# Kernel optimization log

Hardware: AMD Instinct MI355X
Metric: run time of the kernel (lower is better)

Reference implementation:

```python
import jax, jax.numpy as jnp
import numpy as np

N = 50000
E = 600000
FEAT = 32
ACT = 8
H = 128
HEADS = 4
C = H // HEADS
L = 3
NEG_SLOPE = 0.2
LN_EPS = 1e-5


def setup_inputs() -> dict:
    key = jax.random.key(0)
    ks = jax.random.split(key, 32)
    s = 0.05
    inp = {
        'x': jax.random.normal(ks[0], (N, FEAT), jnp.float32),
        'action': jax.random.normal(ks[1], (N, ACT), jnp.float32),
        'edge_index': jax.random.randint(ks[2], (2, E), 0, N, jnp.int32),
        # node encoder: Linear(feat+act -> H) + LayerNorm
        'W0': jax.random.normal(ks[3], (FEAT + ACT, H), jnp.float32) * s,
        'b0': jnp.zeros((H,), jnp.float32),
        'ln0_g': jnp.ones((H,), jnp.float32),
        'ln0_b': jnp.zeros((H,), jnp.float32),
        # GAT layers (stacked over L): lin W [L,H,heads*C], att vectors, bias, LayerNorm
        'Wg': jax.random.normal(ks[4], (L, H, HEADS * C), jnp.float32) * s,
        'att_src': jax.random.normal(ks[5], (L, HEADS, C), jnp.float32) * s,
        'att_dst': jax.random.normal(ks[6], (L, HEADS, C), jnp.float32) * s,
        'bg': jnp.zeros((L, HEADS * C), jnp.float32),
        'lng_g': jnp.ones((L, H), jnp.float32),
        'lng_b': jnp.zeros((L, H), jnp.float32),
        # dynamics head
        'Wd1': jax.random.normal(ks[7], (H, H), jnp.float32) * s,
        'bd1': jnp.zeros((H,), jnp.float32),
        'Wd2': jax.random.normal(ks[8], (H, FEAT), jnp.float32) * s,
        'bd2': jnp.zeros((FEAT,), jnp.float32),
        # reward head
        'Wr1': jax.random.normal(ks[9], (H, H // 2), jnp.float32) * s,
        'br1': jnp.zeros((H // 2,), jnp.float32),
        'Wr2': jax.random.normal(ks[10], (H // 2, 1), jnp.float32) * s,
        'br2': jnp.zeros((1,), jnp.float32),
        # constraint head
        'Wc1': jax.random.normal(ks[11], (H, H // 2), jnp.float32) * s,
        'bc1': jnp.zeros((H // 2,), jnp.float32),
        'Wc2': jax.random.normal(ks[12], (H // 2, 1), jnp.float32) * s,
        'bc2': jnp.zeros((1,), jnp.float32),
    }
    return inp


def _layernorm(x, g, b):
    mu = jnp.mean(x, axis=-1, keepdims=True)
    var = jnp.mean(jnp.square(x - mu), axis=-1, keepdims=True)
    return (x - mu) * jax.lax.rsqrt(var + LN_EPS) * g + b


def _gat_layer(h, src, dst, W, a_src, a_dst, bias):
    # PyG GATConv: xp = lin(h) per head; alpha = leaky_relu(a_src.x_j + a_dst.x_i)
    xp = (h @ W).reshape(N, HEADS, C)                    # [N, heads, C]
    s_src = jnp.sum(xp * a_src, axis=-1)                 # [N, heads]
    s_dst = jnp.sum(xp * a_dst, axis=-1)                 # [N, heads]
    alpha = jax.nn.leaky_relu(s_src[src] + s_dst[dst], NEG_SLOPE)  # [E', heads]
    # segment softmax over edges grouped by destination node
    amax = jax.ops.segment_max(alpha, dst, num_segments=N)
    ex = jnp.exp(alpha - amax[dst])
    den = jax.ops.segment_sum(ex, dst, num_segments=N)
    attn = ex / den[dst]                                 # [E', heads]
    msg = xp[src] * attn[..., None]                      # [E', heads, C]
    out = jax.ops.segment_sum(msg.reshape(-1, HEADS * C), dst, num_segments=N)
    return out + bias                                    # [N, H]


def reference(x, action, edge_index, W0, b0, ln0_g, ln0_b, Wg, att_src, att_dst,
              bg, lng_g, lng_b, Wd1, bd1, Wd2, bd2, Wr1, br1, Wr2, br2,
              Wc1, bc1, Wc2, bc2):
    # add self loops (PyG GATConv default)
    loops = jnp.arange(N, dtype=edge_index.dtype)
    src = jnp.concatenate([edge_index[0], loops])
    dst = jnp.concatenate([edge_index[1], loops])

    h = jax.nn.relu(_layernorm(jnp.concatenate([x, action], axis=-1) @ W0 + b0, ln0_g, ln0_b))
    for l in range(L):
        h_new = _gat_layer(h, src, dst, Wg[l], att_src[l], att_dst[l], bg[l])
        h_new = jax.nn.relu(_layernorm(h_new, lng_g[l], lng_b[l]))
        h = h + h_new

    delta_x = jax.nn.relu(h @ Wd1 + bd1) @ Wd2 + bd2
    next_x = x + delta_x
    graph_emb = jnp.mean(h, axis=0, keepdims=True)       # global_mean_pool, single graph
    reward = (jax.nn.relu(graph_emb @ Wr1 + br1) @ Wr2 + br2).squeeze(-1)
    constraint_prob = jax.nn.sigmoid(jax.nn.relu(graph_emb @ Wc1 + bc1) @ Wc2 + bc2).squeeze(-1)
    return delta_x, next_x, reward, constraint_prob
```

## Files before the change

### kernel.cpp

```cpp
#include <hip/hip_runtime.h>

typedef unsigned short u16;
typedef __attribute__((ext_vector_type(8))) short bf16x8;
typedef __attribute__((ext_vector_type(4))) float f32x4;

#define NN 50000
#define EE 600000
#define EP 650000
#define LNEPS 1e-5f
#define NB 196
#define ENCB 1563
#define CNTB 2540

__device__ __forceinline__ float bf2f(u16 u) {
    union { unsigned int i; float f; } v; v.i = ((unsigned int)u) << 16; return v.f;
}
__device__ __forceinline__ u16 f2bf(float f) {
    union { float f; unsigned int i; } v; v.f = f;
    unsigned int x = v.i;
    unsigned int r = x + 0x7fffu + ((x >> 16) & 1u);
    return (u16)(r >> 16);
}
__device__ __forceinline__ float ldf(const void* p, long i, int bf) {
    return bf ? bf2f(((const u16*)p)[i]) : ((const float*)p)[i];
}
__device__ __forceinline__ void stf(void* p, long i, int bf, float v) {
    if (bf) ((u16*)p)[i] = f2bf(v); else ((float*)p)[i] = v;
}

#define WTOT 93858
#define BSWN 65536
struct P22 { const void* p[22]; };

__global__ __launch_bounds__(256) void init7(P22 w, float* __restrict__ wf,
                                             u16* __restrict__ bsw,
                                             int* __restrict__ deg,
                                             float* __restrict__ gacc,
                                             int* __restrict__ flag) {
    const unsigned w0 = *(const unsigned*)w.p[2];
    const int bf = (w0 == 0x3F803F80u) ? 1 : 0;
    int i = blockIdx.x * 256 + threadIdx.x;
    if (i < WTOT) {
        const int offs[23] = {0,5120,5248,5376,5504,54656,55040,55424,55808,56192,56576,
                              72960,73088,77184,77216,85408,85472,85536,85537,93729,93793,
                              93857,93858};
        int seg = 0;
        while (offs[seg + 1] <= i) ++seg;
        wf[i] = ldf(w.p[seg], i - offs[seg], bf);
        return;
    }
    i -= WTOT;
    if (i < BSWN) {
        int mat = i >> 14, rem = i & 16383;
        int ct = rem >> 11, r2 = rem & 2047;
        int kb = r2 >> 9, r3 = r2 & 511;
        int lane = r3 >> 3, j = r3 & 7;
        int k = kb * 32 + (lane >> 4) * 8 + j;
        int n = ct * 16 + (lane & 15);
        float v = (mat < 3) ? ldf(w.p[4], (long)mat * 16384 + (long)k * 128 + n, bf)
                            : ldf(w.p[10], (long)k * 128 + n, bf);
        bsw[i] = f2bf(v);
        return;
    }
    i -= BSWN;
    if (i < NN) { deg[i] = 0; return; }
    i -= NN;
    if (i < 128) { gacc[i] = 0.f; return; }
    if (i == 128) *flag = bf;
}

__global__ __launch_bounds__(256) void enc7(
    const void* __restrict__ x, const void* __restrict__ act,
    const float* __restrict__ wf, u16* __restrict__ hb,
    const int* __restrict__ flg, const int* __restrict__ ei,
    int* __restrict__ deg) {
    if (blockIdx.x >= ENCB) {
        int e = (blockIdx.x - ENCB) * 256 + threadIdx.x;
        if (e < EP) {
            int d = (e < EE) ? ei[EE + e] : (e - EE);
            atomicAdd(&deg[d], 1);
        }
        return;
    }
    const float* W0f = wf;
    const float* b0f = wf + 5120;
    const float* gf  = wf + 5248;
    const float* bbf = wf + 5376;
    __shared__ float As[32][41];
    const int bf = *flg;
    int t = threadIdx.x;
    int r0 = blockIdx.x * 32;
    #pragma unroll
    for (int i = 0; i < 5; ++i) {
        int idx = t + i * 256;
        int r = idx / 40, k = idx - r * 40;
        int rr = r0 + r; if (rr >= NN) rr = NN - 1;
        As[r][k] = (k < 32) ? ldf(x, (long)rr * 32 + k, bf)
                            : ldf(act, (long)rr * 8 + (k - 32), bf);
    }
    __syncthreads();
    int colq = t & 31, mq = t >> 5;
    int col0 = colq * 4;
    float4 b0v = *(const float4*)(b0f + col0);
    float acc[4][4];
    #pragma unroll
    for (int j = 0; j < 4; ++j) {
        acc[j][0] = b0v.x; acc[j][1] = b0v.y; acc[j][2] = b0v.z; acc[j][3] = b0v.w;
    }
    #pragma unroll 2
    for (int k = 0; k < 40; ++k) {
        float4 b4 = *(const float4*)(W0f + k * 128 + col0);
        float a0 = As[mq * 4 + 0][k];
        float a1 = As[mq * 4 + 1][k];
        float a2 = As[mq * 4 + 2][k];
        float a3 = As[mq * 4 + 3][k];
        acc[0][0] += a0 * b4.x; acc[0][1] += a0 * b4.y; acc[0][2] += a0 * b4.z; acc[0][3] += a0 * b4.w;
        acc[1][0] += a1 * b4.x; acc[1][1] += a1 * b4.y; acc[1][2] += a1 * b4.z; acc[1][3] += a1 * b4.w;
        acc[2][0] += a2 * b4.x; acc[2][1] += a2 * b4.y; acc[2][2] += a2 * b4.z; acc[2][3] += a2 * b4.w;
        acc[3][0] += a3 * b4.x; acc[3][1] += a3 * b4.y; acc[3][2] += a3 * b4.z; acc[3][3] += a3 * b4.w;
    }
    float4 gv = *(const float4*)(gf + col0);
    float4 bv = *(const float4*)(bbf + col0);
    #pragma unroll
    for (int j = 0; j < 4; ++j) {
        int row = r0 + mq * 4 + j;
        float pa = acc[j][0] + acc[j][1] + acc[j][2] + acc[j][3];
        #pragma unroll
        for (int o = 1; o <= 16; o <<= 1) pa += __shfl_xor(pa, o, 32);
        float mu = pa * (1.f / 128.f);
        float d0 = acc[j][0] - mu, d1 = acc[j][1] - mu;
        float d2 = acc[j][2] - mu, d3 = acc[j][3] - mu;
        float q = d0 * d0 + d1 * d1 + d2 * d2 + d3 * d3;
        #pragma unroll
        for (int o = 1; o <= 16; o <<= 1) q += __shfl_xor(q, o, 32);
        float rs = rsqrtf(q * (1.f / 128.f) + LNEPS);
        if (row < NN) {
            ushort4 hbv;
            hbv.x = f2bf(fmaxf(d0 * rs * gv.x + bv.x, 0.f));
            hbv.y = f2bf(fmaxf(d1 * rs * gv.y + bv.y, 0.f));
            hbv.z = f2bf(fmaxf(d2 * rs * gv.z + bv.z, 0.f));
            hbv.w = f2bf(fmaxf(d3 * rs * gv.w + bv.w, 0.f));
            *(ushort4*)(hb + (long)row * 128 + col0) = hbv;
        }
    }
}

__global__ __launch_bounds__(256) void lin7(
    const u16* __restrict__ hb, const u16* __restrict__ bswm,
    const float* __restrict__ bias, u16* __restrict__ out, int dorelu,
    int doscore, const float* __restrict__ wf, int layer,
    float* __restrict__ s_src, float* __restrict__ s_dst,
    int douth, const void* __restrict__ x, void* __restrict__ dout,
    const int* __restrict__ flg) {
    __shared__ u16 As[32 * 136];
    __shared__ u16 ts[32 * 136];
    int t = threadIdx.x;
    int r0 = blockIdx.x * 32;
    #pragma unroll
    for (int i = 0; i < 2; ++i) {
        int idx = (t + i * 256) * 8;
        int r = idx >> 7, k = idx & 127;
        int rr = r0 + r; if (rr >= NN) rr = NN - 1;
        int4 v = *(const int4*)(hb + (long)rr * 128 + k);
        *(int4*)(As + r * 136 + k) = v;
    }
    __syncthreads();
    int w = t >> 6, lane = t & 63;
    int rt = w & 1, ctbase = (w >> 1) * 4;
    int quad = lane >> 4, l15 = lane & 15;
    int rowl = rt * 16 + l15;
    bf16x8 afr[4];
    #pragma unroll
    for (int kb = 0; kb < 4; ++kb)
        afr[kb] = *(const bf16x8*)(As + rowl * 136 + kb * 32 + quad * 8);
    const float* asrf = wf + 54656 + layer * 128;
    const float* adsf = wf + 55040 + layer * 128;
    int headbase = (w >> 1) * 2;
    #pragma unroll
    for (int cp = 0; cp < 2; ++cp) {
        int ct0 = ctbase + cp * 2, ct1 = ct0 + 1;
        f32x4 acc0 = {0.f, 0.f, 0.f, 0.f};
        f32x4 acc1 = {0.f, 0.f, 0.f, 0.f};
        #pragma unroll
        for (int kb = 0; kb < 4; ++kb) {
            bf16x8 b0 = *(const bf16x8*)(bswm + ct0 * 2048 + kb * 512 + lane * 8);
            acc0 = __builtin_amdgcn_mfma_f32_16x16x32_bf16(afr[kb], b0, acc0, 0, 0, 0);
        }
        #pragma unroll
        for (int kb = 0; kb < 4; ++kb) {
            bf16x8 b1 = *(const bf16x8*)(bswm + ct1 * 2048 + kb * 512 + lane * 8);
            acc1 = __builtin_amdgcn_mfma_f32_16x16x32_bf16(afr[kb], b1, acc1, 0, 0, 0);
        }
        int col0 = ct0 * 16 + l15, col1 = ct1 * 16 + l15;
        float bia0 = dorelu ? bias[col0] : 0.f;
        float bia1 = dorelu ? bias[col1] : 0.f;
        #pragma unroll
        for (int reg = 0; reg < 4; ++reg) {
            int lrow = rt * 16 + quad * 4 + reg;
            int grow = r0 + lrow;
            float z0 = acc0[reg] + bia0, z1 = acc1[reg] + bia1;
            if (dorelu) { z0 = fmaxf(z0, 0.f); z1 = fmaxf(z1, 0.f); }
            if (douth) {
                ts[lrow * 136 + col0] = f2bf(z0);
                ts[lrow * 136 + col1] = f2bf(z1);
            } else if (grow < NN) {
                out[(long)grow * 128 + col0] = f2bf(z0);
                out[(long)grow * 128 + col1] = f2bf(z1);
            }
        }
        if (doscore) {
            float av0 = asrf[col0], av1 = asrf[col1];
            float dv0 = adsf[col0], dv1 = adsf[col1];
            #pragma unroll
            for (int reg = 0; reg < 4; ++reg) {
                float pa = acc0[reg] * av0 + acc1[reg] * av1;
                float pb = acc0[reg] * dv0 + acc1[reg] * dv1;
                #pragma unroll
                for (int o = 1; o <= 8; o <<= 1) {
                    pa += __shfl_xor(pa, o, 64);
                    pb += __shfl_xor(pb, o, 64);
                }
                if (l15 == 0) {
                    int grow = r0 + rt * 16 + quad * 4 + reg;
                    if (grow < NN) {
                        s_src[grow * 4 + headbase + cp] = pa;
                        s_dst[grow * 4 + headbase + cp] = pb;
                    }
                }
            }
        }
    }
    if (douth) {
        __syncthreads();
        const float* Wd2f = wf + 73088;
        const float* bd2f = wf + 77184;
        const int bf = *flg;
        int c = t & 31, mq = t >> 5;
        float acc[4];
        #pragma unroll
        for (int j = 0; j < 4; ++j) acc[j] = bd2f[c];
        #pragma unroll 4
        for (int k = 0; k < 128; ++k) {
            float wv = Wd2f[k * 32 + c];
            acc[0] += bf2f(ts[(mq * 4 + 0) * 136 + k]) * wv;
            acc[1] += bf2f(ts[(mq * 4 + 1) * 136 + k]) * wv;
            acc[2] += bf2f(ts[(mq * 4 + 2) * 136 + k]) * wv;
            acc[3] += bf2f(ts[(mq * 4 + 3) * 136 + k]) * wv;
        }
        #pragma unroll
        for (int j = 0; j < 4; ++j) {
            int node = r0 + mq * 4 + j;
            if (node >= NN) continue;
            stf(dout, (long)node * 32 + c, bf, acc[j]);
            stf(dout, (long)NN * 32 + (long)node * 32 + c, bf,
                ldf(x, (long)node * 32 + c, bf) + acc[j]);
        }
    }
}

__global__ __launch_bounds__(256) void scanA(const int* __restrict__ deg,
                                             int* __restrict__ bsum) {
    __shared__ int red[256];
    int t = threadIdx.x; int i = blockIdx.x * 256 + t;
    red[t] = (i < NN) ? deg[i] : 0; __syncthreads();
    for (int s = 128; s >= 1; s >>= 1) { if (t < s) red[t] += red[t + s]; __syncthreads(); }
    if (t == 0) bsum[blockIdx.x] = red[0];
}

__global__ __launch_bounds__(256) void scanC2(const int* __restrict__ deg,
                                              const int* __restrict__ bsum,
                                              int* __restrict__ offs,
                                              int* __restrict__ cursor) {
    __shared__ int sh[256];
    int t = threadIdx.x;
    sh[t] = (t < NB) ? bsum[t] : 0;
    __syncthreads();
    for (int o = 1; o < 256; o <<= 1) {
        int u = (t >= o) ? sh[t - o] : 0;
        __syncthreads();
        sh[t] += u;
        __syncthreads();
    }
    int pre = (blockIdx.x == 0) ? 0 : sh[blockIdx.x - 1];
    __syncthreads();
    int i = blockIdx.x * 256 + t;
    int v = (i < NN) ? deg[i] : 0;
    sh[t] = v;
    __syncthreads();
    for (int o = 1; o < 256; o <<= 1) {
        int u = (t >= o) ? sh[t - o] : 0;
        __syncthreads();
        sh[t] += u;
        __syncthreads();
    }
    if (i < NN) {
        int excl = pre + sh[t] - v;
        offs[i] = excl; cursor[i] = excl;
    }
    if (i == 0) offs[NN] = EP;
}

__global__ void scatter5(const int* __restrict__ ei, int* __restrict__ cursor,
                         int* __restrict__ csrc) {
    int e = blockIdx.x * 256 + threadIdx.x; if (e >= EP) return;
    int s, d;
    if (e < EE) { s = ei[e]; d = ei[EE + e]; } else { s = e - EE; d = s; }
    int p = atomicAdd(&cursor[d], 1);
    csrc[p] = s;
}

__global__ __launch_bounds__(256) void agg10(
    const u16* __restrict__ xp, const float* __restrict__ s_src,
    const float* __restrict__ s_dst,
    const int* __restrict__ csrc, const int* __restrict__ offs,
    const float* __restrict__ wf, int layer, u16* __restrict__ hb) {
    const float* bgf = wf + 55424 + layer * 128;
    const float* gf  = wf + 55808 + layer * 128;
    const float* bbf = wf + 56192 + layer * 128;
    int t = threadIdx.x;
    int lane = t & 63;
    int n = blockIdx.x * 4 + (t >> 6);
    int q = (lane >> 4) & 3;
    int l16 = lane & 15;
    int c0 = l16 * 8;
    int hd = l16 >> 2;
    long idx0 = (long)n * 128 + c0;
    int4 hold = *(const int4*)(hb + idx0);
    float sdn = s_dst[n * 4 + (lane & 3)];
    int beg = offs[n], end = offs[n + 1];
    float a[8] = {};
    float den = 0.f;
    for (int cbeg = beg; cbeg < end; cbeg += 64) {
        int cdeg = end - cbeg; if (cdeg > 64) cdeg = 64;
        int eidx = (lane < cdeg) ? csrc[cbeg + lane] : n;
        for (int base = 0; base < cdeg; base += 16) {
            int me = base + (lane >> 2);
            int sm = __shfl(eidx, me & 63, 64);
            float aw = s_src[sm * 4 + (lane & 3)] + sdn;
            aw = (aw > 0.f) ? aw : 0.2f * aw;
            float wv = (me < cdeg) ? __expf(aw) : 0.f;
            int s00 = __shfl(eidx, base + q, 64);
            int s01 = __shfl(eidx, base + 4 + q, 64);
            int s10 = __shfl(eidx, base + 8 + q, 64);
            int s11 = __shfl(eidx, base + 12 + q, 64);
            int4 v00 = *(const int4*)(xp + (long)s00 * 128 + c0);
            int4 v01 = *(const int4*)(xp + (long)s01 * 128 + c0);
            int4 v10 = *(const int4*)(xp + (long)s10 * 128 + c0);
            int4 v11 = *(const int4*)(xp + (long)s11 * 128 + c0);
            float w00 = __shfl(wv, (q << 2) | hd, 64);
            float w01 = __shfl(wv, ((4 + q) << 2) | hd, 64);
            float w10 = __shfl(wv, ((8 + q) << 2) | hd, 64);
            float w11 = __shfl(wv, ((12 + q) << 2) | hd, 64);
            union { int4 i; u16 u[8]; } u00, u01, u10, u11;
            u00.i = v00; u01.i = v01; u10.i = v10; u11.i = v11;
            #pragma unroll
            for (int k = 0; k < 8; ++k)
                a[k] += w00 * bf2f(u00.u[k]) + w01 * bf2f(u01.u[k])
                      + w10 * bf2f(u10.u[k]) + w11 * bf2f(u11.u[k]);
            den += w00 + w01 + w10 + w11;
        }
    }
    #pragma unroll
    for (int k = 0; k < 8; ++k) {
        a[k] += __shfl_xor(a[k], 16, 64);
        a[k] += __shfl_xor(a[k], 32, 64);
    }
    den += __shfl_xor(den, 16, 64);
    den += __shfl_xor(den, 32, 64);
    float inv = 1.f / den;
    float4 bg0 = *(const float4*)(bgf + c0);
    float4 bg1 = *(const float4*)(bgf + c0 + 4);
    float v[8];
    v[0] = a[0] * inv + bg0.x; v[1] = a[1] * inv + bg0.y;
    v[2] = a[2] * inv + bg0.z; v[3] = a[3] * inv + bg0.w;
    v[4] = a[4] * inv + bg1.x; v[5] = a[5] * inv + bg1.y;
    v[6] = a[6] * inv + bg1.z; v[7] = a[7] * inv + bg1.w;
    float pa = v[0] + v[1] + v[2] + v[3] + v[4] + v[5] + v[6] + v[7];
    #pragma unroll
    for (int o = 1; o <= 8; o <<= 1) pa += __shfl_xor(pa, o, 16);
    float mu = pa * (1.f / 128.f);
    float d[8];
    float qv = 0.f;
    #pragma unroll
    for (int k = 0; k < 8; ++k) { d[k] = v[k] - mu; qv += d[k] * d[k]; }
    #pragma unroll
    for (int o = 1; o <= 8; o <<= 1) qv += __shfl_xor(qv, o, 16);
    float rs = rsqrtf(qv * (1.f / 128.f) + LNEPS);
    float4 g0 = *(const float4*)(gf + c0);
    float4 g1 = *(const float4*)(gf + c0 + 4);
    float4 b0 = *(const float4*)(bbf + c0);
    float4 b1 = *(const float4*)(bbf + c0 + 4);
    float gg[8]  = {g0.x, g0.y, g0.z, g0.w, g1.x, g1.y, g1.z, g1.w};
    float bbv[8] = {b0.x, b0.y, b0.z, b0.w, b1.x, b1.y, b1.z, b1.w};
    if (lane < 16) {
        union { int4 i; u16 u[8]; } hv, ho;
        ho.i = hold;
        #pragma unroll
        for (int k = 0; k < 8; ++k) {
            float y = fmaxf(d[k] * rs * gg[k] + bbv[k], 0.f);
            hv.u[k] = f2bf(bf2f(ho.u[k]) + y);
        }
        *(int4*)(hb + idx0) = hv.i;
    }
}

__global__ __launch_bounds__(128) void pool4(const u16* __restrict__ hb, float* __restrict__ gacc) {
    int c = threadIdx.x;
    int n0 = blockIdx.x * 128;
    float s = 0.f;
    for (int i = 0; i < 128; ++i) {
        int n = n0 + i;
        if (n < NN) s += bf2f(hb[(long)n * 128 + c]);
    }
    atomicAdd(&gacc[c], s);
}

__global__ __launch_bounds__(128) void head4(
    const float* __restrict__ gacc, const float* __restrict__ wf,
    void* __restrict__ out, const int* __restrict__ flg) {
    const float* Wr1f = wf + 77216;
    const float* br1f = wf + 85408;
    const float* Wr2f = wf + 85472;
    const float* br2f = wf + 85536;
    const float* Wc1f = wf + 85537;
    const float* bc1f = wf + 93729;
    const float* Wc2f = wf + 93793;
    const float* bc2f = wf + 93857;
    __shared__ float ge[128];
    __shared__ float hr[128];
    const int bf = *flg;
    int t = threadIdx.x;
    ge[t] = gacc[t] * (1.f / (float)NN);
    __syncthreads();
    {
        int j = t & 63;
        const float* W = (t < 64) ? Wr1f : Wc1f;
        const float* bb = (t < 64) ? br1f : bc1f;
        float a = bb[j];
        for (int k = 0; k < 128; ++k) a += ge[k] * W[k * 64 + j];
        hr[t] = fmaxf(a, 0.f);
    }
    __syncthreads();
    if (t == 0) {
        float r = br2f[0];
        for (int j = 0; j < 64; ++j) r += hr[j] * Wr2f[j];
        stf(out, (long)2 * NN * 32, bf, r);
    } else if (t == 1) {
        float z = bc2f[0];
        for (int j = 0; j < 64; ++j) z += hr[64 + j] * Wc2f[j];
        float p = 1.f / (1.f + __expf(-z));
        stf(out, (long)2 * NN * 32 + 1, bf, p);
    }
}

extern "C" void kernel_launch(void* const* d_in, const int* in_sizes, int n_in,
                              void* d_out, int out_size, void* d_ws, size_t ws_size,
                              hipStream_t stream) {
    const void* x   = d_in[0];
    const void* act = d_in[1];
    const int*  ei  = (const int*)d_in[2];

    char* ws = (char*)d_ws;
    size_t off = 0;
    auto alloc = [&](size_t bytes) -> char* {
        char* p = ws + off;
        off = (off + bytes + 255) & ~(size_t)255;
        return p;
    };
    u16*       hb     = (u16*)      alloc((size_t)NN * 128 * 2);
    u16*       xp     = (u16*)      alloc((size_t)NN * 128 * 2);
    float*     s_src  = (float*)    alloc((size_t)NN * 4 * 4);
    float*     s_dst  = (float*)    alloc((size_t)NN * 4 * 4);
    int*       deg    = (int*)      alloc((size_t)NN * 4);
    int*       cursor = (int*)      alloc((size_t)NN * 4);
    int*       offs   = (int*)      alloc((size_t)(NN + 1) * 4);
    int*       csrc   = (int*)      alloc((size_t)EP * 4);
    float*     wf     = (float*)    alloc((size_t)WTOT * 4);
    u16*       bsw    = (u16*)      alloc((size_t)BSWN * 2);
    float*     gacc   = (float*)    alloc(128 * 4);
    int*       flag   = (int*)      alloc(4);
    int*       bsum   = (int*)      alloc((size_t)NB * 4);
    int*       boff   = (int*)      alloc((size_t)NB * 4);
    (void)boff;

    P22 wp;
    for (int i = 0; i < 22; ++i) wp.p[i] = d_in[3 + i];
    const int initN = WTOT + BSWN + NN + 129;
    init7<<<(initN + 255) / 256, 256, 0, stream>>>(wp, wf, bsw, deg, gacc, flag);

    enc7<<<ENCB + CNTB, 256, 0, stream>>>(x, act, wf, hb, flag, ei, deg);

    scanA<<<NB, 256, 0, stream>>>(deg, bsum);
    scanC2<<<NB, 256, 0, stream>>>(deg, bsum, offs, cursor);
    scatter5<<<(EP + 255) / 256, 256, 0, stream>>>(ei, cursor, csrc);

    for (int l = 0; l < 3; ++l) {
        lin7<<<ENCB, 256, 0, stream>>>(hb, bsw + (size_t)l * 16384,
                                       (const float*)nullptr, xp, 0,
                                       1, wf, l, s_src, s_dst,
                                       0, x, d_out, flag);
        agg10<<<NN / 4, 256, 0, stream>>>(xp, s_src, s_dst, csrc, offs,
                                          wf, l, hb);
    }

    lin7<<<ENCB, 256, 0, stream>>>(hb, bsw + (size_t)3 * 16384,
                                   wf + 72960, xp, 1,
                                   0, wf, 0, s_src, s_dst,
                                   1, x, d_out, flag);

    pool4<<<(NN + 127) / 128, 128, 0, stream>>>(hb, gacc);
    head4<<<1, 128, 0, stream>>>(gacc, wf, d_out, flag);

    (void)in_sizes; (void)n_in; (void)out_size; (void)ws_size;
}
```

Before: 413.3 us.

## Fuse CSR scatter into first GAT linear and pooling into final head linear

The edge scatter that builds the CSR source list now runs as extra blocks inside the first layer's linear kernel, and the global mean-pool partial sums are computed from the shared-memory tile in the final linear kernel. Pooling goes into 16 striped accumulators to spread the atomic traffic, and the head kernel sums them. This removes two kernel launches and a separate pass over the hidden state, at the cost of more atomics inside the final linear and a larger grid for the first linear.

Measured after the change: 377.7 us. -8.6%, faster.

```diff
diff --git a/kernel.cpp b/kernel.cpp
--- a/kernel.cpp
+++ b/kernel.cpp
@@ -65,8 +65,8 @@
     i -= BSWN;
     if (i < NN) { deg[i] = 0; return; }
     i -= NN;
-    if (i < 128) { gacc[i] = 0.f; return; }
-    if (i == 128) *flag = bf;
+    if (i < 2048) { gacc[i] = 0.f; return; }
+    if (i == 2048) *flag = bf;
 }
 
 __global__ __launch_bounds__(256) void enc7(
@@ -145,15 +145,28 @@
     }
 }
 
-__global__ __launch_bounds__(256) void lin7(
+__global__ __launch_bounds__(256) void lin8(
     const u16* __restrict__ hb, const u16* __restrict__ bswm,
     const float* __restrict__ bias, u16* __restrict__ out, int dorelu,
     int doscore, const float* __restrict__ wf, int layer,
     float* __restrict__ s_src, float* __restrict__ s_dst,
     int douth, const void* __restrict__ x, void* __restrict__ dout,
-    const int* __restrict__ flg) {
+    const int* __restrict__ flg,
+    int doscatter, const int* __restrict__ ei, int* __restrict__ cursor,
+    int* __restrict__ csrc, float* __restrict__ gacc) {
+    if (doscatter && blockIdx.x >= ENCB) {
+        int e = (blockIdx.x - ENCB) * 256 + threadIdx.x;
+        if (e < EP) {
+            int s, d;
+            if (e < EE) { s = ei[e]; d = ei[EE + e]; } else { s = e - EE; d = s; }
+            int p = atomicAdd(&cursor[d], 1);
+            csrc[p] = s;
+        }
+        return;
+    }
     __shared__ u16 As[32 * 136];
     __shared__ u16 ts[32 * 136];
+    __shared__ float ps[128];
     int t = threadIdx.x;
     int r0 = blockIdx.x * 32;
     #pragma unroll
@@ -255,6 +268,15 @@
             stf(dout, (long)NN * 32 + (long)node * 32 + c, bf,
                 ldf(x, (long)node * 32 + c, bf) + acc[j]);
         }
+        int pc = t & 127, half = t >> 7;
+        float s = 0.f;
+        #pragma unroll
+        for (int r2 = half * 16; r2 < half * 16 + 16; ++r2) {
+            if (r0 + r2 < NN) s += bf2f(As[r2 * 136 + pc]);
+        }
+        if (half == 0) ps[pc] = s;
+        __syncthreads();
+        if (half == 1) atomicAdd(&gacc[(blockIdx.x & 15) * 128 + pc], s + ps[pc]);
     }
 }
 
@@ -298,15 +320,6 @@
         offs[i] = excl; cursor[i] = excl;
     }
     if (i == 0) offs[NN] = EP;
-}
-
-__global__ void scatter5(const int* __restrict__ ei, int* __restrict__ cursor,
-                         int* __restrict__ csrc) {
-    int e = blockIdx.x * 256 + threadIdx.x; if (e >= EP) return;
-    int s, d;
-    if (e < EE) { s = ei[e]; d = ei[EE + e]; } else { s = e - EE; d = s; }
-    int p = atomicAdd(&cursor[d], 1);
-    csrc[p] = s;
 }
 
 __global__ __launch_bounds__(256) void agg10(
@@ -404,18 +417,7 @@
     }
 }
 
-__global__ __launch_bounds__(128) void pool4(const u16* __restrict__ hb, float* __restrict__ gacc) {
-    int c = threadIdx.x;
-    int n0 = blockIdx.x * 128;
-    float s = 0.f;
-    for (int i = 0; i < 128; ++i) {
-        int n = n0 + i;
-        if (n < NN) s += bf2f(hb[(long)n * 128 + c]);
-    }
-    atomicAdd(&gacc[c], s);
-}
-
-__global__ __launch_bounds__(128) void head4(
+__global__ __launch_bounds__(128) void head5(
     const float* __restrict__ gacc, const float* __restrict__ wf,
     void* __restrict__ out, const int* __restrict__ flg) {
     const float* Wr1f = wf + 77216;
@@ -430,7 +432,12 @@
     __shared__ float hr[128];
     const int bf = *flg;
     int t = threadIdx.x;
-    ge[t] = gacc[t] * (1.f / (float)NN);
+    {
+        float s = 0.f;
+        #pragma unroll
+        for (int k2 = 0; k2 < 16; ++k2) s += gacc[k2 * 128 + t];
+        ge[t] = s * (1.f / (float)NN);
+    }
     __syncthreads();
     {
         int j = t & 63;
@@ -477,39 +484,38 @@
     int*       csrc   = (int*)      alloc((size_t)EP * 4);
     float*     wf     = (float*)    alloc((size_t)WTOT * 4);
     u16*       bsw    = (u16*)      alloc((size_t)BSWN * 2);
-    float*     gacc   = (float*)    alloc(128 * 4);
+    float*     gacc   = (float*)    alloc(16 * 128 * 4);
     int*       flag   = (int*)      alloc(4);
     int*       bsum   = (int*)      alloc((size_t)NB * 4);
-    int*       boff   = (int*)      alloc((size_t)NB * 4);
-    (void)boff;
 
     P22 wp;
     for (int i = 0; i < 22; ++i) wp.p[i] = d_in[3 + i];
-    const int initN = WTOT + BSWN + NN + 129;
+    const int initN = WTOT + BSWN + NN + 2048 + 1;
     init7<<<(initN + 255) / 256, 256, 0, stream>>>(wp, wf, bsw, deg, gacc, flag);
 
     enc7<<<ENCB + CNTB, 256, 0, stream>>>(x, act, wf, hb, flag, ei, deg);
 
     scanA<<<NB, 256, 0, stream>>>(deg, bsum);
     scanC2<<<NB, 256, 0, stream>>>(deg, bsum, offs, cursor);
-    scatter5<<<(EP + 255) / 256, 256, 0, stream>>>(ei, cursor, csrc);
 
     for (int l = 0; l < 3; ++l) {
-        lin7<<<ENCB, 256, 0, stream>>>(hb, bsw + (size_t)l * 16384,
+        int grid = (l == 0) ? (ENCB + CNTB) : ENCB;
+        lin8<<<grid, 256, 0, stream>>>(hb, bsw + (size_t)l * 16384,
                                        (const float*)nullptr, xp, 0,
                                        1, wf, l, s_src, s_dst,
-                                       0, x, d_out, flag);
+                                       0, x, d_out, flag,
+                                       (l == 0) ? 1 : 0, ei, cursor, csrc, gacc);
         agg10<<<NN / 4, 256, 0, stream>>>(xp, s_src, s_dst, csrc, offs,
                                           wf, l, hb);
     }
 
-    lin7<<<ENCB, 256, 0, stream>>>(hb, bsw + (size_t)3 * 16384,
+    lin8<<<ENCB, 256, 0, stream>>>(hb, bsw + (size_t)3 * 16384,
                                    wf + 72960, xp, 1,
                                    0, wf, 0, s_src, s_dst,
-                                   1, x, d_out, flag);
-
-    pool4<<<(NN + 127) / 128, 128, 0, stream>>>(hb, gacc);
-    head4<<<1, 128, 0, stream>>>(gacc, wf, d_out, flag);
+                                   1, x, d_out, flag,
+                                   0, ei, cursor, csrc, gacc);
+
+    head5<<<1, 128, 0, stream>>>(gacc, wf, d_out, flag);
 
     (void)in_sizes; (void)n_in; (void)out_size; (void)ws_size;
 }
```
